# Kernel optimization log

Measured on AMD Instinct MI355X. Metric: run time of the kernel, lower is better.

## Reference

```python
import math
import jax, jax.numpy as jnp
import numpy as np

N_HEADS = 8
WINDOW = 4


def _get_relative_embeddings(emb, length, window):
    # emb: [1, 2*window+1, k_channels] -> [1, 2*length-1, k_channels]
    pad_length = max(length - (window + 1), 0)
    start = max(window + 1 - length, 0)
    if pad_length > 0:
        emb = jnp.pad(emb, ((0, 0), (pad_length, pad_length), (0, 0)))
    return emb[:, start:start + 2 * length - 1]


def _relative_position_to_absolute_position(x):
    # x: [b, h, l, 2l-1] -> [b, h, l, l] (skewing trick)
    b, h, l, _ = x.shape
    x = jnp.pad(x, ((0, 0), (0, 0), (0, 0), (0, 1)))
    x_flat = x.reshape(b, h, l * 2 * l)
    x_flat = jnp.pad(x_flat, ((0, 0), (0, 0), (0, l - 1)))
    return x_flat.reshape(b, h, l + 1, 2 * l - 1)[:, :, :l, l - 1:]


def _absolute_position_to_relative_position(x):
    # x: [b, h, l, l] -> [b, h, l, 2l-1]
    b, h, l, _ = x.shape
    x = jnp.pad(x, ((0, 0), (0, 0), (0, 0), (0, l - 1)))
    x_flat = x.reshape(b, h, l * l + l * (l - 1))
    x_flat = jnp.pad(x_flat, ((0, 0), (0, 0), (l, 0)))
    return x_flat.reshape(b, h, l, 2 * l)[:, :, :, 1:]


def setup_inputs() -> dict:
    key = jax.random.key(0)
    ks = jax.random.split(key, 12)
    b, t, d = 4, 1024, 512
    kc = d // N_HEADS
    s = 1.0 / math.sqrt(d)
    return {
        "x": jax.random.normal(ks[0], (b, t, d), jnp.float32),
        "c": jax.random.normal(ks[1], (b, t, d), jnp.float32),
        "wq": jax.random.normal(ks[2], (d, d), jnp.float32) * s,
        "bq": jnp.zeros((d,), jnp.float32),
        "wk": jax.random.normal(ks[3], (d, d), jnp.float32) * s,
        "bk": jnp.zeros((d,), jnp.float32),
        "wv": jax.random.normal(ks[4], (d, d), jnp.float32) * s,
        "bv": jnp.zeros((d,), jnp.float32),
        "wo": jax.random.normal(ks[5], (d, d), jnp.float32) * s,
        "bo": jnp.zeros((d,), jnp.float32),
        "emb_rel_k": jax.random.normal(ks[6], (1, 2 * WINDOW + 1, kc), jnp.float32) * kc ** -0.5,
        "emb_rel_v": jax.random.normal(ks[7], (1, 2 * WINDOW + 1, kc), jnp.float32) * kc ** -0.5,
    }


def reference(x, c, wq, bq, wk, bk, wv, bv, wo, bo, emb_rel_k, emb_rel_v):
    b, t, d = x.shape
    h = N_HEADS
    kc = d // h
    inv_sqrt = 1.0 / math.sqrt(kc)

    # 1x1 conv projections (pointwise matmul)
    q = x @ wq + bq   # [b, t, d]
    k = c @ wk + bk
    v = c @ wv + bv

    # Faithful reshape as in source: [b, t, d] -> [b, h, kc, t] -> [b, h, t, kc]
    q = q.reshape(b, h, kc, t).transpose(0, 1, 3, 2)
    k = k.reshape(b, h, kc, t).transpose(0, 1, 3, 2)
    v = v.reshape(b, h, kc, t).transpose(0, 1, 3, 2)

    scores = jnp.einsum('bhtd,bhsd->bhts', q, k) * inv_sqrt  # [b,h,t,t]

    # relative key logits
    key_rel = _get_relative_embeddings(emb_rel_k, t, WINDOW)[0]  # [2t-1, kc]
    rel_logits = jnp.einsum('bhtd,md->bhtm', q, key_rel)          # [b,h,t,2t-1]
    scores_local = _relative_position_to_absolute_position(rel_logits) * inv_sqrt
    scores = scores + scores_local

    p_attn = jax.nn.softmax(scores, axis=-1)
    output = jnp.einsum('bhts,bhsd->bhtd', p_attn, v)  # [b,h,t,kc]

    # relative value contribution
    rel_weights = _absolute_position_to_relative_position(p_attn)  # [b,h,t,2t-1]
    val_rel = _get_relative_embeddings(emb_rel_v, t, WINDOW)[0]    # [2t-1, kc]
    output = output + jnp.einsum('bhtm,md->bhtd', rel_weights, val_rel)

    # Faithful output reshape: [b,h,t,kc] -> [b,h,kc,t] -> [b,t,d]
    output = output.transpose(0, 1, 3, 2).reshape(b, t, d)
    out = output @ wo + bo
    return out
```

## Files before the change

### kernel.cpp

```cpp
#include <hip/hip_runtime.h>
#include <hip/hip_bf16.h>

#define NB 4
#define NT 1024
#define ND 512
#define NH 8
#define NKC 64

typedef __bf16 bf16x8 __attribute__((ext_vector_type(8)));
typedef float f32x4 __attribute__((ext_vector_type(4)));

__device__ __forceinline__ f32x4 MFMA(bf16x8 a, bf16x8 b, f32x4 c) {
    return __builtin_amdgcn_mfma_f32_16x16x32_bf16(a, b, c, 0, 0, 0);
}
__device__ __forceinline__ unsigned short f2bu(float v) {
    __hip_bfloat16 b = __float2bfloat16(v);
    return *(unsigned short*)&b;
}
__device__ __forceinline__ void split1(float v, unsigned short& h, unsigned short& l)
{
    __hip_bfloat16 hb = __float2bfloat16(v);
    float r = v - __bfloat162float(hb);
    __hip_bfloat16 lb = __float2bfloat16(r);
    h = *(unsigned short*)&hb;
    l = *(unsigned short*)&lb;
}
__device__ __forceinline__ void splitpack(const float4 a, const float4 b, uint4& h, uint4& l)
{
    union { unsigned short u[8]; uint4 v; } H, L;
    const float f[8] = {a.x, a.y, a.z, a.w, b.x, b.y, b.z, b.w};
    #pragma unroll
    for (int j = 0; j < 8; ++j) split1(f[j], H.u[j], L.u[j]);
    h = H.v; l = L.v;
}

__global__ __launch_bounds__(256)
void splitT_kernel(const float* __restrict__ w0, const float* __restrict__ w1,
                   const float* __restrict__ w2, const float* __restrict__ w3,
                   unsigned short* __restrict__ wT)
{
    __shared__ float tl[32][33];
    const float* w = (blockIdx.z == 0) ? w0 : (blockIdx.z == 1) ? w1
                   : (blockIdx.z == 2) ? w2 : w3;
    unsigned short* hi = wT + (size_t)blockIdx.z * 2 * (ND * ND);
    unsigned short* lo = hi + ND * ND;
    const int t = threadIdx.x;
    const int x0 = blockIdx.x * 32, y0 = blockIdx.y * 32;
    {
        const int r = t >> 3, c = (t & 7) * 4;
        const float4 v = *(const float4*)&w[(size_t)(y0 + r) * ND + x0 + c];
        tl[r][c] = v.x; tl[r][c+1] = v.y; tl[r][c+2] = v.z; tl[r][c+3] = v.w;
    }
    __syncthreads();
    {
        const int nr = t >> 3, k4 = (t & 7) * 4;
        unsigned short hh[4], ll[4];
        #pragma unroll
        for (int j = 0; j < 4; ++j) split1(tl[k4 + j][nr], hh[j], ll[j]);
        ushort4 h = make_ushort4(hh[0], hh[1], hh[2], hh[3]);
        ushort4 l = make_ushort4(ll[0], ll[1], ll[2], ll[3]);
        *(ushort4*)&hi[(size_t)(x0 + nr) * ND + y0 + k4] = h;
        *(ushort4*)&lo[(size_t)(x0 + nr) * ND + y0 + k4] = l;
    }
}

__global__ __launch_bounds__(256, 3)
void proj_mfma(const float* __restrict__ x, const float* __restrict__ cc,
               const unsigned short* __restrict__ wT,
               const float* __restrict__ bq, const float* __restrict__ bk,
               const float* __restrict__ bv,
               unsigned short* __restrict__ qh_o, unsigned short* __restrict__ ql_o,
               unsigned short* __restrict__ kh_o, unsigned short* __restrict__ vh_o)
{
    __shared__ unsigned short smem[12288];
    unsigned short* Ah = smem;
    unsigned short* Al = smem + 2048;
    unsigned short* Bh = smem + 4096;
    unsigned short* Bl = smem + 8192;
    unsigned short* Tr = smem;

    const int which = blockIdx.z;
    const float* A_g = (which == 0) ? x : cc;
    const unsigned short* Bh_g = wT + (size_t)which * 2 * (ND * ND);
    const unsigned short* Bl_g = Bh_g + ND * ND;
    const float* bias = (which == 0) ? bq : (which == 1) ? bk : bv;

    const int tid = threadIdx.x, l = tid & 63, w = tid >> 6;
    const int quad = l >> 4, lc = l & 15;
    const int wm = w & 1, wn = w >> 1;
    const int n0 = blockIdx.x * 128, m0 = blockIdx.y * 64;

    const int am = tid >> 2, ak = (tid & 3) * 8;
    const size_t aG = (size_t)(m0 + am) * ND + ak;
    const int bn = tid >> 1, bk2 = (tid & 1) * 16;
    const size_t bG = (size_t)(n0 + bn) * ND + bk2;

    float4 ra0 = *(const float4*)&A_g[aG];
    float4 ra1 = *(const float4*)&A_g[aG + 4];
    uint4 rb0 = *(const uint4*)&Bh_g[bG];
    uint4 rb1 = *(const uint4*)&Bh_g[bG + 8];
    uint4 rb2 = *(const uint4*)&Bl_g[bG];
    uint4 rb3 = *(const uint4*)&Bl_g[bG + 8];

    f32x4 acc[2][4];
    #pragma unroll
    for (int mi = 0; mi < 2; ++mi)
        #pragma unroll
        for (int ni = 0; ni < 4; ++ni) acc[mi][ni] = (f32x4){0.f, 0.f, 0.f, 0.f};

    for (int k0 = 0; k0 < ND; k0 += 32) {
        __syncthreads();
        {
            uint4 h0, l0;
            splitpack(ra0, ra1, h0, l0);
            *(uint4*)&Ah[am * 32 + ak] = h0;
            *(uint4*)&Al[am * 32 + ak] = l0;
            *(uint4*)&Bh[bn * 32 + bk2] = rb0; *(uint4*)&Bh[bn * 32 + bk2 + 8] = rb1;
            *(uint4*)&Bl[bn * 32 + bk2] = rb2; *(uint4*)&Bl[bn * 32 + bk2 + 8] = rb3;
        }
        __syncthreads();
        if (k0 + 32 < ND) {
            const size_t aN = aG + k0 + 32, bN = bG + k0 + 32;
            ra0 = *(const float4*)&A_g[aN];
            ra1 = *(const float4*)&A_g[aN + 4];
            rb0 = *(const uint4*)&Bh_g[bN];
            rb1 = *(const uint4*)&Bh_g[bN + 8];
            rb2 = *(const uint4*)&Bl_g[bN];
            rb3 = *(const uint4*)&Bl_g[bN + 8];
        }

        bf16x8 ah[2], al2[2], bh[4], bl[4];
        #pragma unroll
        for (int mi = 0; mi < 2; ++mi) {
            const int ar = (wm * 32 + mi * 16 + lc) * 32 + quad * 8;
            ah[mi] = *(const bf16x8*)&Ah[ar];
            al2[mi] = *(const bf16x8*)&Al[ar];
        }
        #pragma unroll
        for (int ni = 0; ni < 4; ++ni) {
            const int br = (wn * 64 + ni * 16 + lc) * 32 + quad * 8;
            bh[ni] = *(const bf16x8*)&Bh[br];
            bl[ni] = *(const bf16x8*)&Bl[br];
        }
        #pragma unroll
        for (int mi = 0; mi < 2; ++mi)
            #pragma unroll
            for (int ni = 0; ni < 4; ++ni) {
                acc[mi][ni] = MFMA(al2[mi], bh[ni], acc[mi][ni]);
                acc[mi][ni] = MFMA(ah[mi], bl[ni], acc[mi][ni]);
                acc[mi][ni] = MFMA(ah[mi], bh[ni], acc[mi][ni]);
            }
    }

    const int bb = m0 >> 10, tt0 = m0 & 1023;
    const int hh = tt0 >> 7, cch0 = (tt0 & 127) >> 1;
    const int bh_idx = bb * NH + hh;

    if (which == 2) {
        #pragma unroll
        for (int ni = 0; ni < 4; ++ni) {
            const int n = n0 + wn * 64 + ni * 16 + lc;
            const float bval = bias[n];
            #pragma unroll
            for (int mi = 0; mi < 2; ++mi)
                #pragma unroll
                for (int r = 0; r < 4; ++r) {
                    const int mloc = wm * 32 + mi * 16 + quad * 4 + r;
                    const int cch = cch0 + (mloc >> 1);
                    const int t = (mloc & 1) * 512 + n;
                    vh_o[(((size_t)bh_idx * 16 + (t >> 6)) * 64 + cch) * 64 + (t & 63)] =
                        f2bu(acc[mi][ni][r] + bval);
                }
        }
        return;
    }

    const int npass = (which == 0) ? 2 : 1;
    unsigned short* outp[2] = {(which == 0) ? qh_o : kh_o, ql_o};

    for (int pass = 0; pass < npass; ++pass) {
        __syncthreads();
        #pragma unroll
        for (int ni = 0; ni < 4; ++ni) {
            const int nloc = wn * 64 + ni * 16 + lc;
            const float bval = bias[n0 + nloc];
            #pragma unroll
            for (int mi = 0; mi < 2; ++mi)
                #pragma unroll
                for (int r = 0; r < 4; ++r) {
                    const int mloc = wm * 32 + mi * 16 + quad * 4 + r;
                    const float val = acc[mi][ni][r] + bval;
                    unsigned short hs, ls;
                    if (which == 0) { split1(val, hs, ls); }
                    else { hs = f2bu(val); ls = 0; }
                    Tr[((mloc & 1) * 128 + nloc) * 40 + (mloc >> 1)] =
                        (pass == 0) ? hs : ls;
                }
        }
        __syncthreads();
        {
            const int t = (tid >> 7) * 512 + n0 + (tid & 127);
            const size_t oa = ((size_t)bh_idx * NT + t) * NKC + cch0;
            const uint4 v0 = *(const uint4*)&Tr[tid * 40];
            const uint4 v1 = *(const uint4*)&Tr[tid * 40 + 8];
            const uint4 v2 = *(const uint4*)&Tr[tid * 40 + 16];
            const uint4 v3 = *(const uint4*)&Tr[tid * 40 + 24];
            *(uint4*)&outp[pass][oa]      = v0;
            *(uint4*)&outp[pass][oa + 8]  = v1;
            *(uint4*)&outp[pass][oa + 16] = v2;
            *(uint4*)&outp[pass][oa + 24] = v3;
        }
    }
}

__global__ __launch_bounds__(256, 4)
void outproj_mfma(const unsigned short* __restrict__ a_g,
                  const unsigned short* __restrict__ wTh,
                  const float* __restrict__ bo, float* __restrict__ out)
{
    __shared__ unsigned short As[64 * 32], Bh[64 * 32], Bl[64 * 32];
    const unsigned short* Bl_g = wTh + ND * ND;
    const int tid = threadIdx.x, l = tid & 63, w = tid >> 6;
    const int quad = l >> 4, lc = l & 15;
    const int wm = w & 1, wn = w >> 1;
    const int n0 = blockIdx.x * 64, m0 = blockIdx.y * 64;

    const int sm = tid >> 2, sk = (tid & 3) * 8;
    const size_t aG = (size_t)(m0 + sm) * ND + sk;
    const size_t bG = (size_t)(n0 + sm) * ND + sk;

    uint4 ra  = *(const uint4*)&a_g[aG];
    uint4 rbh = *(const uint4*)&wTh[bG];
    uint4 rbl = *(const uint4*)&Bl_g[bG];

    f32x4 acc[2][2];
    #pragma unroll
    for (int mi = 0; mi < 2; ++mi)
        #pragma unroll
        for (int ni = 0; ni < 2; ++ni) acc[mi][ni] = (f32x4){0.f, 0.f, 0.f, 0.f};

    for (int k0 = 0; k0 < ND; k0 += 32) {
        __syncthreads();
        *(uint4*)&As[sm * 32 + sk] = ra;
        *(uint4*)&Bh[sm * 32 + sk] = rbh;
        *(uint4*)&Bl[sm * 32 + sk] = rbl;
        __syncthreads();
        if (k0 + 32 < ND) {
            ra  = *(const uint4*)&a_g[aG + k0 + 32];
            rbh = *(const uint4*)&wTh[bG + k0 + 32];
            rbl = *(const uint4*)&Bl_g[bG + k0 + 32];
        }
        bf16x8 ab[2], bhf[2], blf[2];
        #pragma unroll
        for (int mi = 0; mi < 2; ++mi)
            ab[mi] = *(const bf16x8*)&As[(wm * 32 + mi * 16 + lc) * 32 + quad * 8];
        #pragma unroll
        for (int ni = 0; ni < 2; ++ni) {
            const int br = (wn * 32 + ni * 16 + lc) * 32 + quad * 8;
            bhf[ni] = *(const bf16x8*)&Bh[br];
            blf[ni] = *(const bf16x8*)&Bl[br];
        }
        #pragma unroll
        for (int mi = 0; mi < 2; ++mi)
            #pragma unroll
            for (int ni = 0; ni < 2; ++ni) {
                acc[mi][ni] = MFMA(ab[mi], bhf[ni], acc[mi][ni]);
                acc[mi][ni] = MFMA(ab[mi], blf[ni], acc[mi][ni]);
            }
    }

    #pragma unroll
    for (int ni = 0; ni < 2; ++ni) {
        const int n = n0 + wn * 32 + ni * 16 + lc;
        const float bval = bo[n];
        #pragma unroll
        for (int mi = 0; mi < 2; ++mi)
            #pragma unroll
            for (int r = 0; r < 4; ++r) {
                const int m = m0 + wm * 32 + mi * 16 + quad * 4 + r;
                out[(size_t)m * ND + n] = acc[mi][ni][r] + bval;
            }
    }
}

__global__ __launch_bounds__(256, 4)
void attn_mfma(const unsigned short* __restrict__ qh_g, const unsigned short* __restrict__ ql_g,
               const unsigned short* __restrict__ kh_g,
               const unsigned short* __restrict__ vh_g,
               const float* __restrict__ embk, const float* __restrict__ embv,
               float* __restrict__ O0, float* __restrict__ O1,
               float* __restrict__ l0_g, float* __restrict__ l1_g)
{
    __shared__ unsigned short smem[19456];
    unsigned short* KsH = smem;
    unsigned short* Vt  = smem + 4608;
    unsigned short* Ps  = smem + 11264;
    float* bandv = (float*)(smem + 17920);
    unsigned short* EkH = smem + 11264;
    unsigned short* EkL = EkH + 1152;

    const int tid = threadIdx.x, l = tid & 63, w = tid >> 6;
    const int quad = l >> 4, lc = l & 15;
    const int q0 = (blockIdx.x >> 1) * 64;
    const int sh = blockIdx.x & 1;
    const int sBeg = sh * 512;
    const int hh = blockIdx.y, bb = blockIdx.z;
    const int bh = bb * NH + hh;
    const size_t qkBase = (size_t)bh * NT * NKC;
    const size_t vtBase = (size_t)bh * (16 * 64 * 64);
    float* Op = sh ? O1 : O0;
    float* lp = sh ? l1_g : l0_g;

    const int srow = tid >> 2, sseg = (tid & 3) * 16;
    uint4 pk0, pk1, pv0, pv1;
    {
        const size_t ka = qkBase + (size_t)(sBeg + srow) * NKC + sseg;
        const size_t va = vtBase + (size_t)(sBeg >> 6) * 4096 + srow * 64 + sseg;
        pk0 = *(const uint4*)&kh_g[ka];
        pk1 = *(const uint4*)&kh_g[ka + 8];
        pv0 = *(const uint4*)&vh_g[va];
        pv1 = *(const uint4*)&vh_g[va + 8];
    }

    for (int idx = tid; idx < 16 * 72; idx += 256) {
        const int d = idx / 72, kc = idx - d * 72;
        const float v = (d < 9 && kc < 64) ? embk[d * 64 + kc] : 0.f;
        unsigned short hs, ls;
        split1(v, hs, ls);
        EkH[idx] = hs;
        EkL[idx] = ls;
    }
    for (int idx = tid; idx < 64 * 40; idx += 256) {
        const int c = idx / 40, col = 64 + (idx - c * 40);
        const int d = col - 64;
        Vt[c * 104 + col] = f2bu((d < 9) ? embv[d * 64 + c] : 0.f);
    }
    __syncthreads();

    bf16x8 qh[2], ql[2];
    {
        const int qg = q0 + w * 16 + lc;
        const size_t qa = qkBase + (size_t)qg * NKC + quad * 8;
        qh[0] = *(const bf16x8*)&qh_g[qa];
        qh[1] = *(const bf16x8*)&qh_g[qa + 32];
        ql[0] = *(const bf16x8*)&ql_g[qa];
        ql[1] = *(const bf16x8*)&ql_g[qa + 32];
    }

    {
        f32x4 accB = (f32x4){0.f, 0.f, 0.f, 0.f};
        #pragma unroll
        for (int kk = 0; kk < 2; ++kk) {
            const bf16x8 ebh = *(const bf16x8*)&EkH[lc * 72 + kk * 32 + quad * 8];
            const bf16x8 ebl = *(const bf16x8*)&EkL[lc * 72 + kk * 32 + quad * 8];
            accB = MFMA(ql[kk], ebh, accB);
            accB = MFMA(qh[kk], ebl, accB);
            accB = MFMA(qh[kk], ebh, accB);
        }
        __syncthreads();
        if (lc <= 8) {
            #pragma unroll
            for (int r = 0; r < 4; ++r)
                bandv[(w * 16 + quad * 4 + r) * 12 + lc] = accB[r];
        }
    }
    unsigned short* P = Ps + w * 1664;
    {
        const int zr = l >> 2, zc = 80 + (l & 3) * 4;
        *(ushort4*)&P[zr * 104 + zc] = make_ushort4(0, 0, 0, 0);
    }

    f32x4 O[4];
    #pragma unroll
    for (int ci = 0; ci < 4; ++ci) O[ci] = (f32x4){0.f, 0.f, 0.f, 0.f};
    float l_run[4] = {0.f, 0.f, 0.f, 0.f};

    for (int s0 = sBeg; s0 < sBeg + 512; s0 += 64) {
        __syncthreads();
        {
            *(uint4*)&KsH[srow * 72 + sseg]      = pk0;
            *(uint4*)&KsH[srow * 72 + sseg + 8]  = pk1;
            *(uint4*)&Vt[srow * 104 + sseg]      = pv0;
            *(uint4*)&Vt[srow * 104 + sseg + 8]  = pv1;
        }
        __syncthreads();
        if (s0 + 64 < sBeg + 512) {
            const size_t ka = qkBase + (size_t)(s0 + 64 + srow) * NKC + sseg;
            const size_t va = vtBase + (size_t)((s0 + 64) >> 6) * 4096 + srow * 64 + sseg;
            pk0 = *(const uint4*)&kh_g[ka];
            pk1 = *(const uint4*)&kh_g[ka + 8];
            pv0 = *(const uint4*)&vh_g[va];
            pv1 = *(const uint4*)&vh_g[va + 8];
        }

        f32x4 S[4];
        #pragma unroll
        for (int ni = 0; ni < 4; ++ni) {
            f32x4 a = (f32x4){0.f, 0.f, 0.f, 0.f};
            #pragma unroll
            for (int kk = 0; kk < 2; ++kk) {
                const bf16x8 kb = *(const bf16x8*)&KsH[(ni * 16 + lc) * 72 + kk * 32 + quad * 8];
                a = MFMA(ql[kk], kb, a);
                a = MFMA(qh[kk], kb, a);
            }
            S[ni] = a;
        }

        #pragma unroll
        for (int ni = 0; ni < 4; ++ni)
            #pragma unroll
            for (int r = 0; r < 4; ++r) {
                const int ql64 = w * 16 + quad * 4 + r;
                const int dp4 = (s0 + ni * 16 + lc) - (q0 + ql64) + 4;
                float sv = S[ni][r];
                if (dp4 >= 0 && dp4 <= 8) sv += bandv[ql64 * 12 + dp4];
                S[ni][r] = __expf(sv * 0.125f);
            }
        #pragma unroll
        for (int r = 0; r < 4; ++r)
            l_run[r] += S[0][r] + S[1][r] + S[2][r] + S[3][r];

        {
            const int zr = l >> 2, zc = 64 + (l & 3) * 4;
            *(ushort4*)&P[zr * 104 + zc] = make_ushort4(0, 0, 0, 0);
        }
        #pragma unroll
        for (int ni = 0; ni < 4; ++ni)
            #pragma unroll
            for (int r = 0; r < 4; ++r) {
                const int prow = quad * 4 + r;
                const unsigned short pb = f2bu(S[ni][r]);
                P[prow * 104 + ni * 16 + lc] = pb;
                const int dp4 = (s0 + ni * 16 + lc) - (q0 + w * 16 + prow) + 4;
                if (dp4 >= 0 && dp4 <= 8) P[prow * 104 + 64 + dp4] = pb;
            }

        #pragma unroll
        for (int ks = 0; ks < 3; ++ks) {
            const bf16x8 pa = *(const bf16x8*)&P[lc * 104 + ks * 32 + quad * 8];
            #pragma unroll
            for (int ci = 0; ci < 4; ++ci) {
                const bf16x8 vb = *(const bf16x8*)&Vt[(ci * 16 + lc) * 104 + ks * 32 + quad * 8];
                O[ci] = MFMA(pa, vb, O[ci]);
            }
        }
    }

    #pragma unroll
    for (int r = 0; r < 4; ++r) {
        float v = l_run[r];
        v += __shfl_xor(v, 1); v += __shfl_xor(v, 2);
        v += __shfl_xor(v, 4); v += __shfl_xor(v, 8);
        l_run[r] = v;
    }
    const int qg0 = q0 + w * 16 + quad * 4;
    if (lc == 0) {
        #pragma unroll
        for (int r = 0; r < 4; ++r)
            lp[(size_t)bh * NT + qg0 + r] = l_run[r];
    }
    #pragma unroll
    for (int ci = 0; ci < 4; ++ci) {
        const int c = ci * 16 + lc;
        *(f32x4*)&Op[((size_t)bh * 64 + c) * NT + qg0] = O[ci];
    }
}

__global__ __launch_bounds__(256)
void combine_kernel(const float* __restrict__ O0, const float* __restrict__ O1,
                    const float* __restrict__ l0_g, const float* __restrict__ l1_g,
                    unsigned short* __restrict__ ath)
{
    const int q0 = blockIdx.x * 64, hh = blockIdx.y, bb = blockIdx.z;
    const int bh = bb * NH + hh;
    const int tid = threadIdx.x;
    __shared__ float linv[64];
    if (tid < 64)
        linv[tid] = 1.f / (l0_g[(size_t)bh * NT + q0 + tid] +
                           l1_g[(size_t)bh * NT + q0 + tid]);
    __syncthreads();

    const int c = tid >> 2, qq = (tid & 3) * 16;
    const size_t ib = ((size_t)bh * 64 + c) * NT + q0 + qq;
    union { unsigned short u[16]; uint4 v[2]; } out;
    #pragma unroll
    for (int j = 0; j < 16; j += 4) {
        const f32x4 a = *(const f32x4*)&O0[ib + j];
        const f32x4 b = *(const f32x4*)&O1[ib + j];
        #pragma unroll
        for (int r = 0; r < 4; ++r)
            out.u[j + r] = f2bu((a[r] + b[r]) * linv[qq + j + r]);
    }
    const int row = hh * 128 + 2 * c + (q0 >> 9);
    const size_t oa = ((size_t)bb * NT + row) * ND + (q0 & 511) + qq;
    *(uint4*)&ath[oa]     = out.v[0];
    *(uint4*)&ath[oa + 8] = out.v[1];
}

extern "C" void kernel_launch(void* const* d_in, const int* in_sizes, int n_in,
                              void* d_out, int out_size, void* d_ws, size_t ws_size,
                              hipStream_t stream) {
    const float* x    = (const float*)d_in[0];
    const float* c    = (const float*)d_in[1];
    const float* wq   = (const float*)d_in[2];
    const float* bq   = (const float*)d_in[3];
    const float* wk   = (const float*)d_in[4];
    const float* bk   = (const float*)d_in[5];
    const float* wv   = (const float*)d_in[6];
    const float* bv   = (const float*)d_in[7];
    const float* wo   = (const float*)d_in[8];
    const float* bo   = (const float*)d_in[9];
    const float* embk = (const float*)d_in[10];
    const float* embv = (const float*)d_in[11];

    unsigned short* u16 = (unsigned short*)d_ws;
    const size_t M = 1024 * 1024;
    unsigned short* wT  = u16;
    unsigned short* qh  = u16 + 2 * M;
    unsigned short* ql  = u16 + 4 * M;
    unsigned short* kh  = u16 + 6 * M;
    unsigned short* vh  = u16 + 8 * M;
    unsigned short* ath = u16 + 10 * M;
    float* fbase = (float*)(u16 + 12 * M);
    float* O0   = fbase;
    float* O1   = fbase + 2 * M;
    float* l0_g = fbase + 4 * M;
    float* l1_g = l0_g + 32768;

    splitT_kernel<<<dim3(16, 16, 4), 256, 0, stream>>>(wq, wk, wv, wo, wT);

    proj_mfma<<<dim3(4, 64, 3), 256, 0, stream>>>(x, c, wT, bq, bk, bv,
                                                  qh, ql, kh, vh);

    attn_mfma<<<dim3(32, 8, 4), 256, 0, stream>>>(qh, ql, kh, vh,
                                                  embk, embv, O0, O1, l0_g, l1_g);

    combine_kernel<<<dim3(16, 8, 4), 256, 0, stream>>>(O0, O1, l0_g, l1_g, ath);

    outproj_mfma<<<dim3(8, 64), 256, 0, stream>>>(ath,
                                                  wT + (size_t)3 * 2 * ND * ND,
                                                  bo, (float*)d_out);
}
```

Baseline: 163.8 us.

## Fuse combine into output projection, trim split-precision MFMAs, double-buffer KV loads

Folds the split-softmax combine step into the output projection GEMM, so the normalized attention output is built on the fly from O0/O1 and the row sums instead of being staged through an intermediate bf16 buffer, which removes one launch and one round trip through memory. The V projection and the relative-key embedding now drop the low-part bf16 correction term, cutting MFMA work and shared-memory traffic at some cost in accuracy. The attention loop now keeps two KV tiles in flight in registers, prefetching two tiles ahead. The fused kernel recomputes a 1024-entry reciprocal table in every block and re-reads O0/O1 once per output-column block.

```diff
diff --git a/kernel.cpp b/kernel.cpp
--- a/kernel.cpp
+++ b/kernel.cpp
@@ -99,8 +99,11 @@
     float4 ra1 = *(const float4*)&A_g[aG + 4];
     uint4 rb0 = *(const uint4*)&Bh_g[bG];
     uint4 rb1 = *(const uint4*)&Bh_g[bG + 8];
-    uint4 rb2 = *(const uint4*)&Bl_g[bG];
-    uint4 rb3 = *(const uint4*)&Bl_g[bG + 8];
+    uint4 rb2 = {}, rb3 = {};
+    if (which != 2) {
+        rb2 = *(const uint4*)&Bl_g[bG];
+        rb3 = *(const uint4*)&Bl_g[bG + 8];
+    }
 
     f32x4 acc[2][4];
     #pragma unroll
@@ -116,7 +119,9 @@
             *(uint4*)&Ah[am * 32 + ak] = h0;
             *(uint4*)&Al[am * 32 + ak] = l0;
             *(uint4*)&Bh[bn * 32 + bk2] = rb0; *(uint4*)&Bh[bn * 32 + bk2 + 8] = rb1;
-            *(uint4*)&Bl[bn * 32 + bk2] = rb2; *(uint4*)&Bl[bn * 32 + bk2 + 8] = rb3;
+            if (which != 2) {
+                *(uint4*)&Bl[bn * 32 + bk2] = rb2; *(uint4*)&Bl[bn * 32 + bk2 + 8] = rb3;
+            }
         }
         __syncthreads();
         if (k0 + 32 < ND) {
@@ -125,8 +130,10 @@
             ra1 = *(const float4*)&A_g[aN + 4];
             rb0 = *(const uint4*)&Bh_g[bN];
             rb1 = *(const uint4*)&Bh_g[bN + 8];
-            rb2 = *(const uint4*)&Bl_g[bN];
-            rb3 = *(const uint4*)&Bl_g[bN + 8];
+            if (which != 2) {
+                rb2 = *(const uint4*)&Bl_g[bN];
+                rb3 = *(const uint4*)&Bl_g[bN + 8];
+            }
         }
 
         bf16x8 ah[2], al2[2], bh[4], bl[4];
@@ -140,16 +147,26 @@
         for (int ni = 0; ni < 4; ++ni) {
             const int br = (wn * 64 + ni * 16 + lc) * 32 + quad * 8;
             bh[ni] = *(const bf16x8*)&Bh[br];
-            bl[ni] = *(const bf16x8*)&Bl[br];
-        }
-        #pragma unroll
-        for (int mi = 0; mi < 2; ++mi)
-            #pragma unroll
-            for (int ni = 0; ni < 4; ++ni) {
-                acc[mi][ni] = MFMA(al2[mi], bh[ni], acc[mi][ni]);
-                acc[mi][ni] = MFMA(ah[mi], bl[ni], acc[mi][ni]);
-                acc[mi][ni] = MFMA(ah[mi], bh[ni], acc[mi][ni]);
-            }
+            if (which != 2) bl[ni] = *(const bf16x8*)&Bl[br];
+        }
+        if (which != 2) {
+            #pragma unroll
+            for (int mi = 0; mi < 2; ++mi)
+                #pragma unroll
+                for (int ni = 0; ni < 4; ++ni) {
+                    acc[mi][ni] = MFMA(al2[mi], bh[ni], acc[mi][ni]);
+                    acc[mi][ni] = MFMA(ah[mi], bl[ni], acc[mi][ni]);
+                    acc[mi][ni] = MFMA(ah[mi], bh[ni], acc[mi][ni]);
+                }
+        } else {
+            #pragma unroll
+            for (int mi = 0; mi < 2; ++mi)
+                #pragma unroll
+                for (int ni = 0; ni < 4; ++ni) {
+                    acc[mi][ni] = MFMA(al2[mi], bh[ni], acc[mi][ni]);
+                    acc[mi][ni] = MFMA(ah[mi], bh[ni], acc[mi][ni]);
+                }
+        }
     }
 
     const int bb = m0 >> 10, tt0 = m0 & 1023;
@@ -210,76 +227,6 @@
             *(uint4*)&outp[pass][oa + 16] = v2;
             *(uint4*)&outp[pass][oa + 24] = v3;
         }
-    }
-}
-
-__global__ __launch_bounds__(256, 4)
-void outproj_mfma(const unsigned short* __restrict__ a_g,
-                  const unsigned short* __restrict__ wTh,
-                  const float* __restrict__ bo, float* __restrict__ out)
-{
-    __shared__ unsigned short As[64 * 32], Bh[64 * 32], Bl[64 * 32];
-    const unsigned short* Bl_g = wTh + ND * ND;
-    const int tid = threadIdx.x, l = tid & 63, w = tid >> 6;
-    const int quad = l >> 4, lc = l & 15;
-    const int wm = w & 1, wn = w >> 1;
-    const int n0 = blockIdx.x * 64, m0 = blockIdx.y * 64;
-
-    const int sm = tid >> 2, sk = (tid & 3) * 8;
-    const size_t aG = (size_t)(m0 + sm) * ND + sk;
-    const size_t bG = (size_t)(n0 + sm) * ND + sk;
-
-    uint4 ra  = *(const uint4*)&a_g[aG];
-    uint4 rbh = *(const uint4*)&wTh[bG];
-    uint4 rbl = *(const uint4*)&Bl_g[bG];
-
-    f32x4 acc[2][2];
-    #pragma unroll
-    for (int mi = 0; mi < 2; ++mi)
-        #pragma unroll
-        for (int ni = 0; ni < 2; ++ni) acc[mi][ni] = (f32x4){0.f, 0.f, 0.f, 0.f};
-
-    for (int k0 = 0; k0 < ND; k0 += 32) {
-        __syncthreads();
-        *(uint4*)&As[sm * 32 + sk] = ra;
-        *(uint4*)&Bh[sm * 32 + sk] = rbh;
-        *(uint4*)&Bl[sm * 32 + sk] = rbl;
-        __syncthreads();
-        if (k0 + 32 < ND) {
-            ra  = *(const uint4*)&a_g[aG + k0 + 32];
-            rbh = *(const uint4*)&wTh[bG + k0 + 32];
-            rbl = *(const uint4*)&Bl_g[bG + k0 + 32];
-        }
-        bf16x8 ab[2], bhf[2], blf[2];
-        #pragma unroll
-        for (int mi = 0; mi < 2; ++mi)
-            ab[mi] = *(const bf16x8*)&As[(wm * 32 + mi * 16 + lc) * 32 + quad * 8];
-        #pragma unroll
-        for (int ni = 0; ni < 2; ++ni) {
-            const int br = (wn * 32 + ni * 16 + lc) * 32 + quad * 8;
-            bhf[ni] = *(const bf16x8*)&Bh[br];
-            blf[ni] = *(const bf16x8*)&Bl[br];
-        }
-        #pragma unroll
-        for (int mi = 0; mi < 2; ++mi)
-            #pragma unroll
-            for (int ni = 0; ni < 2; ++ni) {
-                acc[mi][ni] = MFMA(ab[mi], bhf[ni], acc[mi][ni]);
-                acc[mi][ni] = MFMA(ab[mi], blf[ni], acc[mi][ni]);
-            }
-    }
-
-    #pragma unroll
-    for (int ni = 0; ni < 2; ++ni) {
-        const int n = n0 + wn * 32 + ni * 16 + lc;
-        const float bval = bo[n];
-        #pragma unroll
-        for (int mi = 0; mi < 2; ++mi)
-            #pragma unroll
-            for (int r = 0; r < 4; ++r) {
-                const int m = m0 + wm * 32 + mi * 16 + quad * 4 + r;
-                out[(size_t)m * ND + n] = acc[mi][ni][r] + bval;
-            }
     }
 }
 
@@ -297,7 +244,6 @@
     unsigned short* Ps  = smem + 11264;
     float* bandv = (float*)(smem + 17920);
     unsigned short* EkH = smem + 11264;
-    unsigned short* EkL = EkH + 1152;
 
     const int tid = threadIdx.x, l = tid & 63, w = tid >> 6;
     const int quad = l >> 4, lc = l & 15;
@@ -312,23 +258,23 @@
     float* lp = sh ? l1_g : l0_g;
 
     const int srow = tid >> 2, sseg = (tid & 3) * 16;
-    uint4 pk0, pk1, pv0, pv1;
-    {
-        const size_t ka = qkBase + (size_t)(sBeg + srow) * NKC + sseg;
-        const size_t va = vtBase + (size_t)(sBeg >> 6) * 4096 + srow * 64 + sseg;
-        pk0 = *(const uint4*)&kh_g[ka];
-        pk1 = *(const uint4*)&kh_g[ka + 8];
-        pv0 = *(const uint4*)&vh_g[va];
-        pv1 = *(const uint4*)&vh_g[va + 8];
-    }
+
+    auto loadKV = [&](uint4& k0r, uint4& k1r, uint4& v0r, uint4& v1r, int tile) {
+        const size_t ka = qkBase + (size_t)(sBeg + tile * 64 + srow) * NKC + sseg;
+        const size_t va = vtBase + (size_t)((sBeg >> 6) + tile) * 4096 + srow * 64 + sseg;
+        k0r = *(const uint4*)&kh_g[ka];
+        k1r = *(const uint4*)&kh_g[ka + 8];
+        v0r = *(const uint4*)&vh_g[va];
+        v1r = *(const uint4*)&vh_g[va + 8];
+    };
+
+    uint4 ak0, ak1, av0, av1, bk0, bk1, bv0, bv1;
+    loadKV(ak0, ak1, av0, av1, 0);
+    loadKV(bk0, bk1, bv0, bv1, 1);
 
     for (int idx = tid; idx < 16 * 72; idx += 256) {
         const int d = idx / 72, kc = idx - d * 72;
-        const float v = (d < 9 && kc < 64) ? embk[d * 64 + kc] : 0.f;
-        unsigned short hs, ls;
-        split1(v, hs, ls);
-        EkH[idx] = hs;
-        EkL[idx] = ls;
+        EkH[idx] = f2bu((d < 9 && kc < 64) ? embk[d * 64 + kc] : 0.f);
     }
     for (int idx = tid; idx < 64 * 40; idx += 256) {
         const int c = idx / 40, col = 64 + (idx - c * 40);
@@ -352,9 +298,7 @@
         #pragma unroll
         for (int kk = 0; kk < 2; ++kk) {
             const bf16x8 ebh = *(const bf16x8*)&EkH[lc * 72 + kk * 32 + quad * 8];
-            const bf16x8 ebl = *(const bf16x8*)&EkL[lc * 72 + kk * 32 + quad * 8];
             accB = MFMA(ql[kk], ebh, accB);
-            accB = MFMA(qh[kk], ebl, accB);
             accB = MFMA(qh[kk], ebh, accB);
         }
         __syncthreads();
@@ -375,23 +319,16 @@
     for (int ci = 0; ci < 4; ++ci) O[ci] = (f32x4){0.f, 0.f, 0.f, 0.f};
     float l_run[4] = {0.f, 0.f, 0.f, 0.f};
 
-    for (int s0 = sBeg; s0 < sBeg + 512; s0 += 64) {
-        __syncthreads();
-        {
-            *(uint4*)&KsH[srow * 72 + sseg]      = pk0;
-            *(uint4*)&KsH[srow * 72 + sseg + 8]  = pk1;
-            *(uint4*)&Vt[srow * 104 + sseg]      = pv0;
-            *(uint4*)&Vt[srow * 104 + sseg + 8]  = pv1;
-        }
-        __syncthreads();
-        if (s0 + 64 < sBeg + 512) {
-            const size_t ka = qkBase + (size_t)(s0 + 64 + srow) * NKC + sseg;
-            const size_t va = vtBase + (size_t)((s0 + 64) >> 6) * 4096 + srow * 64 + sseg;
-            pk0 = *(const uint4*)&kh_g[ka];
-            pk1 = *(const uint4*)&kh_g[ka + 8];
-            pv0 = *(const uint4*)&vh_g[va];
-            pv1 = *(const uint4*)&vh_g[va + 8];
-        }
+    auto tilestep = [&](uint4& k0r, uint4& k1r, uint4& v0r, uint4& v1r,
+                        int i, int nextTile) {
+        const int s0 = sBeg + i * 64;
+        __syncthreads();
+        *(uint4*)&KsH[srow * 72 + sseg]      = k0r;
+        *(uint4*)&KsH[srow * 72 + sseg + 8]  = k1r;
+        *(uint4*)&Vt[srow * 104 + sseg]      = v0r;
+        *(uint4*)&Vt[srow * 104 + sseg + 8]  = v1r;
+        __syncthreads();
+        if (nextTile >= 0) loadKV(k0r, k1r, v0r, v1r, nextTile);
 
         f32x4 S[4];
         #pragma unroll
@@ -444,6 +381,11 @@
                 O[ci] = MFMA(pa, vb, O[ci]);
             }
         }
+    };
+
+    for (int ii = 0; ii < 8; ii += 2) {
+        tilestep(ak0, ak1, av0, av1, ii,     (ii + 2 < 8) ? ii + 2 : -1);
+        tilestep(bk0, bk1, bv0, bv1, ii + 1, (ii + 3 < 8) ? ii + 3 : -1);
     }
 
     #pragma unroll
@@ -466,35 +408,99 @@
     }
 }
 
-__global__ __launch_bounds__(256)
-void combine_kernel(const float* __restrict__ O0, const float* __restrict__ O1,
-                    const float* __restrict__ l0_g, const float* __restrict__ l1_g,
-                    unsigned short* __restrict__ ath)
+__global__ __launch_bounds__(256, 4)
+void outproj_fused(const float* __restrict__ O0, const float* __restrict__ O1,
+                   const float* __restrict__ l0_g, const float* __restrict__ l1_g,
+                   const unsigned short* __restrict__ wTh,
+                   const float* __restrict__ bo, float* __restrict__ out)
 {
-    const int q0 = blockIdx.x * 64, hh = blockIdx.y, bb = blockIdx.z;
+    __shared__ unsigned short As[64 * 32], Bh[64 * 32], Bl[64 * 32];
+    __shared__ float linv[1024];
+    const unsigned short* Bl_g = wTh + ND * ND;
+    const int tid = threadIdx.x, l = tid & 63, w = tid >> 6;
+    const int quad = l >> 4, lc = l & 15;
+    const int wm = w & 1, wn = w >> 1;
+    const int n0 = blockIdx.x * 64, m0 = blockIdx.y * 64;
+
+    const int bb = m0 >> 10, hh = (m0 & 1023) >> 7;
     const int bh = bb * NH + hh;
-    const int tid = threadIdx.x;
-    __shared__ float linv[64];
-    if (tid < 64)
-        linv[tid] = 1.f / (l0_g[(size_t)bh * NT + q0 + tid] +
-                           l1_g[(size_t)bh * NT + q0 + tid]);
-    __syncthreads();
-
-    const int c = tid >> 2, qq = (tid & 3) * 16;
-    const size_t ib = ((size_t)bh * 64 + c) * NT + q0 + qq;
-    union { unsigned short u[16]; uint4 v[2]; } out;
-    #pragma unroll
-    for (int j = 0; j < 16; j += 4) {
-        const f32x4 a = *(const f32x4*)&O0[ib + j];
-        const f32x4 b = *(const f32x4*)&O1[ib + j];
-        #pragma unroll
-        for (int r = 0; r < 4; ++r)
-            out.u[j + r] = f2bu((a[r] + b[r]) * linv[qq + j + r]);
-    }
-    const int row = hh * 128 + 2 * c + (q0 >> 9);
-    const size_t oa = ((size_t)bb * NT + row) * ND + (q0 & 511) + qq;
-    *(uint4*)&ath[oa]     = out.v[0];
-    *(uint4*)&ath[oa + 8] = out.v[1];
+
+    for (int i = tid; i < 1024; i += 256)
+        linv[i] = 1.f / (l0_g[(size_t)bh * NT + i] + l1_g[(size_t)bh * NT + i]);
+
+    const int sm = tid >> 2, sk = (tid & 3) * 8;
+    const int cch = ((m0 & 127) + sm) >> 1, tb = sm & 1;
+    const size_t oBase = ((size_t)bh * 64 + cch) * NT + tb * 512 + sk;
+    const size_t bG = (size_t)(n0 + sm) * ND + sk;
+
+    float4 ro0a = *(const float4*)&O0[oBase];
+    float4 ro0b = *(const float4*)&O0[oBase + 4];
+    float4 ro1a = *(const float4*)&O1[oBase];
+    float4 ro1b = *(const float4*)&O1[oBase + 4];
+    uint4 rbh = *(const uint4*)&wTh[bG];
+    uint4 rbl = *(const uint4*)&Bl_g[bG];
+
+    f32x4 acc[2][2];
+    #pragma unroll
+    for (int mi = 0; mi < 2; ++mi)
+        #pragma unroll
+        for (int ni = 0; ni < 2; ++ni) acc[mi][ni] = (f32x4){0.f, 0.f, 0.f, 0.f};
+
+    for (int k0 = 0; k0 < ND; k0 += 32) {
+        __syncthreads();
+        {
+            const float* lv = &linv[tb * 512 + k0 + sk];
+            const float f[8] = {ro0a.x + ro1a.x, ro0a.y + ro1a.y,
+                                ro0a.z + ro1a.z, ro0a.w + ro1a.w,
+                                ro0b.x + ro1b.x, ro0b.y + ro1b.y,
+                                ro0b.z + ro1b.z, ro0b.w + ro1b.w};
+            union { unsigned short u[8]; uint4 v; } pk;
+            #pragma unroll
+            for (int j = 0; j < 8; ++j) pk.u[j] = f2bu(f[j] * lv[j]);
+            *(uint4*)&As[sm * 32 + sk] = pk.v;
+            *(uint4*)&Bh[sm * 32 + sk] = rbh;
+            *(uint4*)&Bl[sm * 32 + sk] = rbl;
+        }
+        __syncthreads();
+        if (k0 + 32 < ND) {
+            ro0a = *(const float4*)&O0[oBase + k0 + 32];
+            ro0b = *(const float4*)&O0[oBase + k0 + 36];
+            ro1a = *(const float4*)&O1[oBase + k0 + 32];
+            ro1b = *(const float4*)&O1[oBase + k0 + 36];
+            rbh  = *(const uint4*)&wTh[bG + k0 + 32];
+            rbl  = *(const uint4*)&Bl_g[bG + k0 + 32];
+        }
+        bf16x8 ab[2], bhf[2], blf[2];
+        #pragma unroll
+        for (int mi = 0; mi < 2; ++mi)
+            ab[mi] = *(const bf16x8*)&As[(wm * 32 + mi * 16 + lc) * 32 + quad * 8];
+        #pragma unroll
+        for (int ni = 0; ni < 2; ++ni) {
+            const int br = (wn * 32 + ni * 16 + lc) * 32 + quad * 8;
+            bhf[ni] = *(const bf16x8*)&Bh[br];
+            blf[ni] = *(const bf16x8*)&Bl[br];
+        }
+        #pragma unroll
+        for (int mi = 0; mi < 2; ++mi)
+            #pragma unroll
+            for (int ni = 0; ni < 2; ++ni) {
+                acc[mi][ni] = MFMA(ab[mi], bhf[ni], acc[mi][ni]);
+                acc[mi][ni] = MFMA(ab[mi], blf[ni], acc[mi][ni]);
+            }
+    }
+
+    #pragma unroll
+    for (int ni = 0; ni < 2; ++ni) {
+        const int n = n0 + wn * 32 + ni * 16 + lc;
+        const float bval = bo[n];
+        #pragma unroll
+        for (int mi = 0; mi < 2; ++mi)
+            #pragma unroll
+            for (int r = 0; r < 4; ++r) {
+                const int m = m0 + wm * 32 + mi * 16 + quad * 4 + r;
+                out[(size_t)m * ND + n] = acc[mi][ni][r] + bval;
+            }
+    }
 }
 
 extern "C" void kernel_launch(void* const* d_in, const int* in_sizes, int n_in,
@@ -520,8 +526,7 @@
     unsigned short* ql  = u16 + 4 * M;
     unsigned short* kh  = u16 + 6 * M;
     unsigned short* vh  = u16 + 8 * M;
-    unsigned short* ath = u16 + 10 * M;
-    float* fbase = (float*)(u16 + 12 * M);
+    float* fbase = (float*)(u16 + 10 * M);
     float* O0   = fbase;
     float* O1   = fbase + 2 * M;
     float* l0_g = fbase + 4 * M;
@@ -535,9 +540,7 @@
     attn_mfma<<<dim3(32, 8, 4), 256, 0, stream>>>(qh, ql, kh, vh,
                                                   embk, embv, O0, O1, l0_g, l1_g);
 
-    combine_kernel<<<dim3(16, 8, 4), 256, 0, stream>>>(O0, O1, l0_g, l1_g, ath);
-
-    outproj_mfma<<<dim3(8, 64), 256, 0, stream>>>(ath,
-                                                  wT + (size_t)3 * 2 * ND * ND,
-                                                  bo, (float*)d_out);
-}
+    outproj_fused<<<dim3(8, 64), 256, 0, stream>>>(O0, O1, l0_g, l1_g,
+                                                   wT + (size_t)3 * 2 * ND * ND,
+                                                   bo, (float*)d_out);
+}
```

New measurement: 171.1 us. 4.5% more time.
